# Kernel tuning notes

Hardware: AMD Instinct MI355X
Metric: run time of the kernel (lower is better)

## Reference

```python
import jax, jax.numpy as jnp
import numpy as np

NHEADS = 16


def setup_inputs() -> dict:
    key = jax.random.key(0)
    ks = jax.random.split(key, 5)
    B, S, D = 2, 2048, 1024
    x = jax.random.normal(ks[0], (B, S, D), dtype=jnp.float32)
    W_packed = jax.random.normal(ks[1], (3 * D, D), dtype=jnp.float32) * (1.0 / np.sqrt(D))
    b_packed = jax.random.normal(ks[2], (3 * D,), dtype=jnp.float32) * 0.02
    W_out = jax.random.normal(ks[3], (D, D), dtype=jnp.float32) * (1.0 / np.sqrt(D))
    b_out = jax.random.normal(ks[4], (D,), dtype=jnp.float32) * 0.02
    return {"x": x, "W_packed": W_packed, "b_packed": b_packed, "W_out": W_out, "b_out": b_out}


def reference(x, W_packed, b_packed, W_out, b_out):
    B, S, D = x.shape
    H = NHEADS
    hd = D // H
    # packed QKV projection (self-attention: q is k is v)
    qkv = x @ W_packed.T + b_packed                       # [B,S,3D]
    q, k, v = jnp.split(qkv, 3, axis=-1)

    def heads(t):
        return t.reshape(B, S, H, hd).transpose(0, 2, 1, 3)  # [B,H,S,hd]

    q, k, v = map(heads, (q, k, v))

    # ALiBi slopes per flex path: exp2(-(h+1)*8/H)
    slopes = jnp.exp2(-(jnp.arange(1, H + 1, dtype=x.dtype) * (8.0 / H)))  # [H]
    pos = jnp.arange(S)
    rel = (pos[None, :] - pos[:, None]).astype(x.dtype)    # kv_idx - q_idx, [S,S]
    bias = slopes[:, None, None] * rel                     # [H,S,S]
    causal = pos[None, :] <= pos[:, None]                  # allowed positions
    neg = jnp.finfo(x.dtype).min
    attn_mask = jnp.where(causal[None, :, :], bias, neg)   # [H,S,S]

    scale = 1.0 / np.sqrt(hd)
    scores = jnp.einsum("bhqd,bhkd->bhqk", q, k) * scale + attn_mask[None]
    attn = jax.nn.softmax(scores, axis=-1)
    out = jnp.einsum("bhqk,bhkd->bhqd", attn, v)           # [B,H,S,hd]
    out = out.transpose(0, 2, 1, 3).reshape(B, S, D)
    return out @ W_out.T + b_out
```

## Files before the change

### kernel.cpp

```cpp
#include <hip/hip_runtime.h>

typedef float f32x4 __attribute__((ext_vector_type(4)));
typedef __bf16 bf16x8 __attribute__((ext_vector_type(8)));
typedef unsigned short u16;

__device__ __forceinline__ f32x4 mfma16(bf16x8 a, bf16x8 b, f32x4 c) {
  return __builtin_amdgcn_mfma_f32_16x16x32_bf16(a, b, c, 0, 0, 0);
}

__device__ __forceinline__ int pidx16(int row, int kc) {
  return ((((row >> 6) * 32 + (kc >> 2)) * 4 + ((row >> 4) & 3)) << 6) +
         ((kc & 3) << 4) + (row & 15);
}

__global__ void cvt3_kernel(const float* __restrict__ x,
                            const float* __restrict__ wp,
                            const float* __restrict__ wo,
                            u16* __restrict__ apx, u16* __restrict__ bpx,
                            u16* __restrict__ wox) {
  int idx = blockIdx.x * blockDim.x + threadIdx.x;
  int stride = gridDim.x * blockDim.x;
  for (int i = idx; i < 1048576; i += stride) {
    const float* src;
    u16* dst;
    int j;
    if (i < 524288) {
      j = i; src = x + (size_t)j * 8; dst = apx;
    } else if (i < 917504) {
      j = i - 524288; src = wp + (size_t)j * 8; dst = bpx;
    } else {
      j = i - 917504; src = wo + (size_t)j * 8; dst = wox;
    }
    f32x4 a = *(const f32x4*)src;
    f32x4 b = *(const f32x4*)(src + 4);
    bf16x8 r;
#pragma unroll
    for (int e = 0; e < 4; ++e) {
      r[e] = (__bf16)a[e];
      r[4 + e] = (__bf16)b[e];
    }
    int row = j >> 7, kc = j & 127;
    *(bf16x8*)(dst + (size_t)pidx16(row, kc) * 8) = r;
  }
}

template <int NREP, int MODE>
__global__ __launch_bounds__(256, 2) void gemm_frag(
    const u16* __restrict__ apx, const u16* __restrict__ bpx,
    const float* __restrict__ bias, float* __restrict__ Cout,
    __bf16* __restrict__ qb, __bf16* __restrict__ kp, __bf16* __restrict__ vp,
    int N) {
  const int tid = threadIdx.x;
  const int wid = tid >> 6;
  const int lane = tid & 63;
  const int lr = lane & 15, lg = lane >> 4;

  const int lid = blockIdx.x;
  const int xcd = lid & 7;
  const int local = lid >> 3;
  const int mib = xcd * 2 + (local & 1);
  const int nj = local >> 1;
  const int mi64 = mib * 4 + wid;

  const u16* ab = apx + (size_t)mi64 * 65536 + lane * 8;
  const u16* bb;
  int colbase;
  if (NREP == 4) {
    bb = bpx + (size_t)nj * 65536 + lane * 8;
    colbase = nj * 64;
  } else {
    bb = bpx + (size_t)(nj >> 1) * 65536 + (nj & 1) * 1024 + lane * 8;
    colbase = nj * 32;
  }

  f32x4 acc[4][NREP] = {};
  bf16x8 a0[4], b0[NREP], a1[4], b1[NREP];
#pragma unroll
  for (int mt = 0; mt < 4; ++mt) a0[mt] = *(const bf16x8*)(ab + mt * 512);
#pragma unroll
  for (int nt = 0; nt < NREP; ++nt) b0[nt] = *(const bf16x8*)(bb + nt * 512);

  for (int kt = 0; kt < 32; kt += 2) {
#pragma unroll
    for (int mt = 0; mt < 4; ++mt)
      a1[mt] = *(const bf16x8*)(ab + (kt + 1) * 2048 + mt * 512);
#pragma unroll
    for (int nt = 0; nt < NREP; ++nt)
      b1[nt] = *(const bf16x8*)(bb + (kt + 1) * 2048 + nt * 512);
#pragma unroll
    for (int mt = 0; mt < 4; ++mt)
#pragma unroll
      for (int nt = 0; nt < NREP; ++nt)
        acc[mt][nt] = mfma16(a0[mt], b0[nt], acc[mt][nt]);
    if (kt + 2 < 32) {
#pragma unroll
      for (int mt = 0; mt < 4; ++mt)
        a0[mt] = *(const bf16x8*)(ab + (kt + 2) * 2048 + mt * 512);
#pragma unroll
      for (int nt = 0; nt < NREP; ++nt)
        b0[nt] = *(const bf16x8*)(bb + (kt + 2) * 2048 + nt * 512);
    }
#pragma unroll
    for (int mt = 0; mt < 4; ++mt)
#pragma unroll
      for (int nt = 0; nt < NREP; ++nt)
        acc[mt][nt] = mfma16(a1[mt], b1[nt], acc[mt][nt]);
  }

#pragma unroll
  for (int nt = 0; nt < NREP; ++nt) {
    int col = colbase + nt * 16 + lr;
    float bv = bias[col];
#pragma unroll
    for (int mt = 0; mt < 4; ++mt) {
#pragma unroll
      for (int r = 0; r < 4; ++r) {
        int row = mi64 * 64 + mt * 16 + lg * 4 + r;
        float val = acc[mt][nt][r] + bv;
        if (MODE == 0) {
          Cout[(size_t)row * N + col] = val;
        } else {
          __bf16 bx = (__bf16)val;
          int b = row >> 11, s = row & 2047;
          int third = col >> 10, hd = col & 1023;
          int h = hd >> 6, d = hd & 63;
          if (third == 0) {
            qb[(size_t)row * 1024 + hd] = bx;
          } else {
            int bh = b * 16 + h, t2 = s >> 6, sr = s & 63;
            size_t tb = ((size_t)(bh * 32 + t2)) * 4096;
            if (third == 1)
              kp[tb + (sr >> 4) * 1024 + (d >> 5) * 512 + ((d >> 3) & 3) * 128 +
                 (sr & 15) * 8 + (d & 7)] = bx;
            else
              vp[tb + (d >> 4) * 1024 + (sr >> 5) * 512 + ((sr >> 3) & 3) * 128 +
                 (d & 15) * 8 + (sr & 7)] = bx;
          }
        }
      }
    }
  }
}

__global__ __launch_bounds__(64, 4) void attn_kernel(
    const __bf16* __restrict__ qb, const __bf16* __restrict__ kp,
    const __bf16* __restrict__ vp, u16* __restrict__ abp) {
  __shared__ __bf16 p_lds[16][72];
  const int lane = threadIdx.x & 63;
  const int lr = lane & 15;
  const int lg = lane >> 4;

  const int lid = blockIdx.x;
  const int xcd = lid & 7;
  const int rest = lid >> 3;
  const int bh = xcd * 4 + (rest & 3);
  const int a16 = 127 - (rest >> 2);
  const int b = bh >> 4, h = bh & 15;
  const int qr0 = a16 * 16;
  const int ntl = (a16 >> 2) + 1;

  const float LOG2E = 1.4426950408889634f;
  const float c1 = 0.125f * LOG2E;
  const float c2 = exp2f(-(float)(h + 1) * 0.5f) * LOG2E;

  bf16x8 ones;
#pragma unroll
  for (int j = 0; j < 8; ++j) ones[j] = (__bf16)1.0f;

  const u16* ktiles = (const u16*)kp + (size_t)bh * 32 * 4096;
  const u16* vtiles = (const u16*)vp + (size_t)bh * 32 * 4096;

  const __bf16* qrow = qb + (size_t)(b * 2048 + qr0 + lr) * 1024 + h * 64;
  bf16x8 qf0 = *(const bf16x8*)(qrow + lg * 8);
  bf16x8 qf1 = *(const bf16x8*)(qrow + 32 + lg * 8);

  float m[4], l[4], cq[4];
  f32x4 o[4];
#pragma unroll
  for (int r = 0; r < 4; ++r) {
    m[r] = 0.f;
    l[r] = 0.f;
    cq[r] = c2 * (float)(qr0 + lg * 4 + r);
  }
#pragma unroll
  for (int dt = 0; dt < 4; ++dt) o[dt] = (f32x4){0.f, 0.f, 0.f, 0.f};

  for (int t = 0; t < ntl; ++t) {
    const u16* kb = ktiles + (size_t)t * 4096;
    const u16* vb = vtiles + (size_t)t * 4096;
    const int kv = t * 64;
    const bool last = (t == ntl - 1);

    bf16x8 ka[8], va[8];
#pragma unroll
    for (int j = 0; j < 8; ++j)
      ka[j] = *(const bf16x8*)(kb + j * 512 + lane * 8);
#pragma unroll
    for (int j = 0; j < 8; ++j)
      va[j] = *(const bf16x8*)(vb + j * 512 + lane * 8);

    f32x4 s[4];
#pragma unroll
    for (int nt = 0; nt < 4; ++nt) {
      f32x4 tt = (f32x4){0.f, 0.f, 0.f, 0.f};
      tt = mfma16(qf0, ka[nt * 2], tt);
      tt = mfma16(qf1, ka[nt * 2 + 1], tt);
      s[nt] = tt;
    }

#pragma unroll
    for (int nt = 0; nt < 4; ++nt) {
      float bnt = c2 * (float)(kv + nt * 16 + lr);
#pragma unroll
      for (int r = 0; r < 4; ++r)
        s[nt][r] = __builtin_fmaf(s[nt][r], c1, bnt - cq[r]);
    }
    if (last) {
#pragma unroll
      for (int nt = 0; nt < 4; ++nt) {
        float kf = (float)(kv + nt * 16 + lr);
#pragma unroll
        for (int r = 0; r < 4; ++r) {
          float qi = (float)(qr0 + lg * 4 + r);
          if (kf > qi) s[nt][r] = -1e30f;
        }
      }
    }

    float pm[4];
#pragma unroll
    for (int r = 0; r < 4; ++r)
      pm[r] = fmaxf(fmaxf(s[0][r], s[1][r]), fmaxf(s[2][r], s[3][r]));
    bool ok = (pm[0] <= m[0] + 8.f) && (pm[1] <= m[1] + 8.f) &&
              (pm[2] <= m[2] + 8.f) && (pm[3] <= m[3] + 8.f);
    if (!__all(ok)) {
#pragma unroll
      for (int r = 0; r < 4; ++r)
#pragma unroll
        for (int d = 1; d < 16; d <<= 1)
          pm[r] = fmaxf(pm[r], __shfl_xor(pm[r], d));
#pragma unroll
      for (int r = 0; r < 4; ++r) {
        float mn = fmaxf(m[r], pm[r]);
        float fac = __builtin_amdgcn_exp2f(m[r] - mn);
        m[r] = mn;
        l[r] *= fac;
#pragma unroll
        for (int dt = 0; dt < 4; ++dt) o[dt][r] *= fac;
      }
    }

#pragma unroll
    for (int nt = 0; nt < 4; ++nt)
#pragma unroll
      for (int r = 0; r < 4; ++r) {
        float e = __builtin_amdgcn_exp2f(s[nt][r] - m[r]);
        p_lds[lg * 4 + r][nt * 16 + lr] = (__bf16)e;
      }

    bf16x8 pa0 = *(const bf16x8*)&p_lds[lr][lg * 8];
    bf16x8 pa1 = *(const bf16x8*)&p_lds[lr][32 + lg * 8];

    {
      f32x4 tt = (f32x4){0.f, 0.f, 0.f, 0.f};
      tt = mfma16(pa0, ones, tt);
      tt = mfma16(pa1, ones, tt);
#pragma unroll
      for (int r = 0; r < 4; ++r) l[r] += tt[r];
    }

#pragma unroll
    for (int dt = 0; dt < 4; ++dt) {
      o[dt] = mfma16(pa0, va[dt * 2], o[dt]);
      o[dt] = mfma16(pa1, va[dt * 2 + 1], o[dt]);
    }
  }

  const int mi_g = b * 32 + (a16 >> 2);
#pragma unroll
  for (int dt = 0; dt < 4; ++dt)
#pragma unroll
    for (int r = 0; r < 4; ++r) {
      float val = o[dt][r] / l[r];
      __bf16 bx = (__bf16)val;
      int off16 = (((mi_g * 32 + h * 2 + (dt >> 1)) * 4 + (a16 & 3)) << 6) +
                  (((dt & 1) * 2 + (lr >> 3)) << 4) + lg * 4 + r;
      abp[(size_t)off16 * 8 + (lr & 7)] = *(u16*)&bx;
    }
}

extern "C" void kernel_launch(void* const* d_in, const int* in_sizes, int n_in,
                              void* d_out, int out_size, void* d_ws, size_t ws_size,
                              hipStream_t stream) {
  (void)in_sizes; (void)n_in; (void)out_size; (void)ws_size;
  const float* x = (const float*)d_in[0];
  const float* Wp = (const float*)d_in[1];
  const float* bp = (const float*)d_in[2];
  const float* Wo = (const float*)d_in[3];
  const float* bo = (const float*)d_in[4];
  float* out = (float*)d_out;

  char* ws = (char*)d_ws;
  u16* apx = (u16*)(ws);
  u16* bpx = (u16*)(ws + (size_t)(8u << 20));
  u16* wox = (u16*)(ws + (size_t)(14u << 20));
  u16* qbp = (u16*)(ws + (size_t)(16u << 20));
  u16* kpp = (u16*)(ws + (size_t)(24u << 20));
  u16* vpp = (u16*)(ws + (size_t)(32u << 20));
  u16* abp = (u16*)(ws + (size_t)(40u << 20));

  cvt3_kernel<<<2048, 256, 0, stream>>>(x, Wp, Wo, apx, bpx, wox);
  gemm_frag<4, 1><<<768, 256, 0, stream>>>(
      apx, bpx, bp, nullptr, (__bf16*)qbp, (__bf16*)kpp, (__bf16*)vpp, 3072);
  attn_kernel<<<4096, 64, 0, stream>>>(
      (const __bf16*)qbp, (const __bf16*)kpp, (const __bf16*)vpp, abp);
  gemm_frag<2, 0><<<512, 256, 0, stream>>>(
      abp, wox, bo, out, nullptr, nullptr, nullptr, 1024);
}
```

Before: 119.6 us.

## Replace QKV projection GEMM with LDS-staged 256x256 tiled kernel

The QKV projection GEMM moves from a register-only fragment-layout kernel to a 512-thread, 256x256-tile kernel. It stages A and B tiles into double-buffered LDS using global_load_lds with an XOR swizzle, and interleaves staging of quarter-tiles with four MFMA phases using barriers and setprio. The conversion kernel now writes x and W_packed as plain row-major bf16 instead of the pre-permuted fragment layout. The intent is more operand reuse per global byte and better overlap of loads with MFMA, at the cost of many more barriers and a grid of only 192 workgroups.

```diff
diff --git a/kernel.cpp b/kernel.cpp
--- a/kernel.cpp
+++ b/kernel.cpp
@@ -8,6 +8,12 @@
   return __builtin_amdgcn_mfma_f32_16x16x32_bf16(a, b, c, 0, 0, 0);
 }
 
+__device__ __forceinline__ void gll16(const void* g, void* l) {
+  __builtin_amdgcn_global_load_lds(
+      (const __attribute__((address_space(1))) void*)g,
+      (__attribute__((address_space(3))) void*)l, 16, 0, 0);
+}
+
 __device__ __forceinline__ int pidx16(int row, int kc) {
   return ((((row >> 6) * 32 + (kc >> 2)) * 4 + ((row >> 4) & 3)) << 6) +
          ((kc & 3) << 4) + (row & 15);
@@ -16,21 +22,17 @@
 __global__ void cvt3_kernel(const float* __restrict__ x,
                             const float* __restrict__ wp,
                             const float* __restrict__ wo,
-                            u16* __restrict__ apx, u16* __restrict__ bpx,
+                            __bf16* __restrict__ xb, __bf16* __restrict__ wpb,
                             u16* __restrict__ wox) {
   int idx = blockIdx.x * blockDim.x + threadIdx.x;
   int stride = gridDim.x * blockDim.x;
   for (int i = idx; i < 1048576; i += stride) {
     const float* src;
-    u16* dst;
     int j;
-    if (i < 524288) {
-      j = i; src = x + (size_t)j * 8; dst = apx;
-    } else if (i < 917504) {
-      j = i - 524288; src = wp + (size_t)j * 8; dst = bpx;
-    } else {
-      j = i - 917504; src = wo + (size_t)j * 8; dst = wox;
-    }
+    int mode;
+    if (i < 524288) { j = i; src = x + (size_t)j * 8; mode = 0; }
+    else if (i < 917504) { j = i - 524288; src = wp + (size_t)j * 8; mode = 1; }
+    else { j = i - 917504; src = wo + (size_t)j * 8; mode = 2; }
     f32x4 a = *(const f32x4*)src;
     f32x4 b = *(const f32x4*)(src + 4);
     bf16x8 r;
@@ -39,83 +41,173 @@
       r[e] = (__bf16)a[e];
       r[4 + e] = (__bf16)b[e];
     }
-    int row = j >> 7, kc = j & 127;
-    *(bf16x8*)(dst + (size_t)pidx16(row, kc) * 8) = r;
-  }
-}
-
-template <int NREP, int MODE>
-__global__ __launch_bounds__(256, 2) void gemm_frag(
-    const u16* __restrict__ apx, const u16* __restrict__ bpx,
+    if (mode == 0) *(bf16x8*)(xb + (size_t)j * 8) = r;
+    else if (mode == 1) *(bf16x8*)(wpb + (size_t)j * 8) = r;
+    else {
+      int row = j >> 7, kc = j & 127;
+      *(bf16x8*)(wox + (size_t)pidx16(row, kc) * 8) = r;
+    }
+  }
+}
+
+template <int MODE>
+__global__ __launch_bounds__(512, 2) void gemm8p(
+    const u16* __restrict__ A, const u16* __restrict__ B,
     const float* __restrict__ bias, float* __restrict__ Cout,
     __bf16* __restrict__ qb, __bf16* __restrict__ kp, __bf16* __restrict__ vp,
-    int N) {
+    int N, int K, int mtiles) {
+  __shared__ u16 lA[2 * 256 * 64];
+  __shared__ u16 lB[2 * 256 * 64];
   const int tid = threadIdx.x;
   const int wid = tid >> 6;
   const int lane = tid & 63;
   const int lr = lane & 15, lg = lane >> 4;
 
+  const int nwg = gridDim.x;
   const int lid = blockIdx.x;
-  const int xcd = lid & 7;
-  const int local = lid >> 3;
-  const int mib = xcd * 2 + (local & 1);
-  const int nj = local >> 1;
-  const int mi64 = mib * 4 + wid;
-
-  const u16* ab = apx + (size_t)mi64 * 65536 + lane * 8;
-  const u16* bb;
-  int colbase;
-  if (NREP == 4) {
-    bb = bpx + (size_t)nj * 65536 + lane * 8;
-    colbase = nj * 64;
-  } else {
-    bb = bpx + (size_t)(nj >> 1) * 65536 + (nj & 1) * 1024 + lane * 8;
-    colbase = nj * 32;
-  }
-
-  f32x4 acc[4][NREP] = {};
-  bf16x8 a0[4], b0[NREP], a1[4], b1[NREP];
-#pragma unroll
-  for (int mt = 0; mt < 4; ++mt) a0[mt] = *(const bf16x8*)(ab + mt * 512);
-#pragma unroll
-  for (int nt = 0; nt < NREP; ++nt) b0[nt] = *(const bf16x8*)(bb + nt * 512);
-
-  for (int kt = 0; kt < 32; kt += 2) {
-#pragma unroll
-    for (int mt = 0; mt < 4; ++mt)
-      a1[mt] = *(const bf16x8*)(ab + (kt + 1) * 2048 + mt * 512);
-#pragma unroll
-    for (int nt = 0; nt < NREP; ++nt)
-      b1[nt] = *(const bf16x8*)(bb + (kt + 1) * 2048 + nt * 512);
-#pragma unroll
-    for (int mt = 0; mt < 4; ++mt)
-#pragma unroll
-      for (int nt = 0; nt < NREP; ++nt)
-        acc[mt][nt] = mfma16(a0[mt], b0[nt], acc[mt][nt]);
-    if (kt + 2 < 32) {
-#pragma unroll
-      for (int mt = 0; mt < 4; ++mt)
-        a0[mt] = *(const bf16x8*)(ab + (kt + 2) * 2048 + mt * 512);
-#pragma unroll
-      for (int nt = 0; nt < NREP; ++nt)
-        b0[nt] = *(const bf16x8*)(bb + (kt + 2) * 2048 + nt * 512);
-    }
-#pragma unroll
-    for (int mt = 0; mt < 4; ++mt)
-#pragma unroll
-      for (int nt = 0; nt < NREP; ++nt)
-        acc[mt][nt] = mfma16(a1[mt], b1[nt], acc[mt][nt]);
-  }
-
-#pragma unroll
-  for (int nt = 0; nt < NREP; ++nt) {
-    int col = colbase + nt * 16 + lr;
+  const int sw = (lid & 7) * (nwg >> 3) + (lid >> 3);
+  const int bm = (sw % mtiles) * 256;
+  const int bn = (sw / mtiles) * 256;
+  const int wm = (wid >> 2) * 128;
+  const int wn = (wid & 3) * 64;
+
+  f32x4 acc[8][4] = {};
+  const int KT = K >> 6;
+  const int NH = KT * 4;
+
+  auto stageh = [&](int h) {
+    if (h >= NH) return;
+    const int kt = h >> 2, part = h & 3, slot = kt & 1;
+    const int kk = kt << 6;
+#pragma unroll
+    for (int j = 0; j < 2; ++j) {
+      int o16 = tid + j * 512;
+      int rl = o16 >> 3;
+      int gcol = (((o16 & 7) ^ (rl & 7)) << 3);
+      if (part < 2)
+        gll16(A + (size_t)(bm + part * 128 + rl) * K + kk + gcol,
+              (char*)lA + slot * 32768 + part * 16384 + o16 * 16);
+      else
+        gll16(B + (size_t)(bn + (part - 2) * 128 + rl) * K + kk + gcol,
+              (char*)lB + slot * 32768 + (part - 2) * 16384 + o16 * 16);
+    }
+  };
+
+  auto rdA = [&](int slot, int mt, int ks) -> bf16x8 {
+    int row = wm + mt * 16 + lr;
+    int col = ((ks * 4 + lg) ^ (row & 7)) << 3;
+    return *(const bf16x8*)&lA[slot * 16384 + row * 64 + col];
+  };
+  auto rdB = [&](int slot, int nt, int ks) -> bf16x8 {
+    int row = wn + nt * 16 + lr;
+    int col = ((ks * 4 + lg) ^ (row & 7)) << 3;
+    return *(const bf16x8*)&lB[slot * 16384 + row * 64 + col];
+  };
+
+#pragma unroll
+  for (int h = 0; h < 5; ++h) stageh(h);
+  asm volatile("s_waitcnt vmcnt(2)" ::: "memory");
+  __builtin_amdgcn_s_barrier();
+
+  bf16x8 afA[4][2], afB[4][2], bfA[2][2], bfB[2][2];
+  for (int kt = 0; kt < KT; ++kt) {
+    const int slot = kt & 1;
+    const int hb = (kt + 1) * 4;
+#pragma unroll
+    for (int mt = 0; mt < 4; ++mt) {
+      afA[mt][0] = rdA(slot, mt, 0);
+      afA[mt][1] = rdA(slot, mt, 1);
+    }
+#pragma unroll
+    for (int nt = 0; nt < 2; ++nt) {
+      bfA[nt][0] = rdB(slot, nt, 0);
+      bfA[nt][1] = rdB(slot, nt, 1);
+    }
+    stageh(hb + 1);
+    __builtin_amdgcn_sched_barrier(0);
+    __builtin_amdgcn_s_barrier();
+    asm volatile("s_waitcnt lgkmcnt(0)" ::: "memory");
+    __builtin_amdgcn_sched_barrier(0);
+    __builtin_amdgcn_s_setprio(1);
+#pragma unroll
+    for (int mt = 0; mt < 4; ++mt)
+#pragma unroll
+      for (int nt = 0; nt < 2; ++nt)
+#pragma unroll
+        for (int ks = 0; ks < 2; ++ks)
+          acc[mt][nt] = mfma16(afA[mt][ks], bfA[nt][ks], acc[mt][nt]);
+    __builtin_amdgcn_s_setprio(0);
+    __builtin_amdgcn_sched_barrier(0);
+    __builtin_amdgcn_s_barrier();
+#pragma unroll
+    for (int nt = 0; nt < 2; ++nt) {
+      bfB[nt][0] = rdB(slot, nt + 2, 0);
+      bfB[nt][1] = rdB(slot, nt + 2, 1);
+    }
+    stageh(hb + 2);
+    __builtin_amdgcn_sched_barrier(0);
+    __builtin_amdgcn_s_barrier();
+    asm volatile("s_waitcnt lgkmcnt(0)" ::: "memory");
+    __builtin_amdgcn_sched_barrier(0);
+    __builtin_amdgcn_s_setprio(1);
+#pragma unroll
+    for (int mt = 0; mt < 4; ++mt)
+#pragma unroll
+      for (int nt = 0; nt < 2; ++nt)
+#pragma unroll
+        for (int ks = 0; ks < 2; ++ks)
+          acc[mt][nt + 2] = mfma16(afA[mt][ks], bfB[nt][ks], acc[mt][nt + 2]);
+    __builtin_amdgcn_s_setprio(0);
+    __builtin_amdgcn_sched_barrier(0);
+    __builtin_amdgcn_s_barrier();
+#pragma unroll
+    for (int mt = 0; mt < 4; ++mt) {
+      afB[mt][0] = rdA(slot, mt + 4, 0);
+      afB[mt][1] = rdA(slot, mt + 4, 1);
+    }
+    stageh(hb + 3);
+    __builtin_amdgcn_sched_barrier(0);
+    __builtin_amdgcn_s_barrier();
+    asm volatile("s_waitcnt lgkmcnt(0)" ::: "memory");
+    __builtin_amdgcn_sched_barrier(0);
+    __builtin_amdgcn_s_setprio(1);
+#pragma unroll
+    for (int mt = 0; mt < 4; ++mt)
+#pragma unroll
+      for (int nt = 0; nt < 2; ++nt)
+#pragma unroll
+        for (int ks = 0; ks < 2; ++ks)
+          acc[mt + 4][nt] = mfma16(afB[mt][ks], bfA[nt][ks], acc[mt + 4][nt]);
+    __builtin_amdgcn_s_setprio(0);
+    __builtin_amdgcn_sched_barrier(0);
+    __builtin_amdgcn_s_barrier();
+    stageh(hb + 4);
+    __builtin_amdgcn_sched_barrier(0);
+    __builtin_amdgcn_s_barrier();
+    __builtin_amdgcn_s_setprio(1);
+#pragma unroll
+    for (int mt = 0; mt < 4; ++mt)
+#pragma unroll
+      for (int nt = 0; nt < 2; ++nt)
+#pragma unroll
+        for (int ks = 0; ks < 2; ++ks)
+          acc[mt + 4][nt + 2] =
+              mfma16(afB[mt][ks], bfB[nt][ks], acc[mt + 4][nt + 2]);
+    __builtin_amdgcn_s_setprio(0);
+    __builtin_amdgcn_sched_barrier(0);
+    asm volatile("s_waitcnt vmcnt(2)" ::: "memory");
+    __builtin_amdgcn_s_barrier();
+  }
+
+#pragma unroll
+  for (int nt = 0; nt < 4; ++nt) {
+    int col = bn + wn + nt * 16 + lr;
     float bv = bias[col];
 #pragma unroll
-    for (int mt = 0; mt < 4; ++mt) {
+    for (int mt = 0; mt < 8; ++mt) {
 #pragma unroll
       for (int r = 0; r < 4; ++r) {
-        int row = mi64 * 64 + mt * 16 + lg * 4 + r;
+        int row = bm + wm + mt * 16 + lg * 4 + r;
         float val = acc[mt][nt][r] + bv;
         if (MODE == 0) {
           Cout[(size_t)row * N + col] = val;
@@ -142,6 +234,82 @@
   }
 }
 
+template <int NREP, int MODE>
+__global__ __launch_bounds__(256, 2) void gemm_frag(
+    const u16* __restrict__ apx, const u16* __restrict__ bpx,
+    const float* __restrict__ bias, float* __restrict__ Cout, int N) {
+  const int tid = threadIdx.x;
+  const int wid = tid >> 6;
+  const int lane = tid & 63;
+  const int lr = lane & 15, lg = lane >> 4;
+
+  const int lid = blockIdx.x;
+  const int xcd = lid & 7;
+  const int local = lid >> 3;
+  const int mib = xcd * 2 + (local & 1);
+  const int nj = local >> 1;
+  const int mi64 = mib * 4 + wid;
+
+  const u16* ab = apx + (size_t)mi64 * 65536 + lane * 8;
+  const u16* bb;
+  int colbase;
+  if (NREP == 4) {
+    bb = bpx + (size_t)nj * 65536 + lane * 8;
+    colbase = nj * 64;
+  } else {
+    bb = bpx + (size_t)(nj >> 1) * 65536 + (nj & 1) * 1024 + lane * 8;
+    colbase = nj * 32;
+  }
+
+  f32x4 acc[4][NREP] = {};
+  bf16x8 a0[4], b0[NREP], a1[4], b1[NREP];
+#pragma unroll
+  for (int mt = 0; mt < 4; ++mt) a0[mt] = *(const bf16x8*)(ab + mt * 512);
+#pragma unroll
+  for (int nt = 0; nt < NREP; ++nt) b0[nt] = *(const bf16x8*)(bb + nt * 512);
+
+  for (int kt = 0; kt < 32; kt += 2) {
+#pragma unroll
+    for (int mt = 0; mt < 4; ++mt)
+      a1[mt] = *(const bf16x8*)(ab + (kt + 1) * 2048 + mt * 512);
+#pragma unroll
+    for (int nt = 0; nt < NREP; ++nt)
+      b1[nt] = *(const bf16x8*)(bb + (kt + 1) * 2048 + nt * 512);
+#pragma unroll
+    for (int mt = 0; mt < 4; ++mt)
+#pragma unroll
+      for (int nt = 0; nt < NREP; ++nt)
+        acc[mt][nt] = mfma16(a0[mt], b0[nt], acc[mt][nt]);
+    if (kt + 2 < 32) {
+#pragma unroll
+      for (int mt = 0; mt < 4; ++mt)
+        a0[mt] = *(const bf16x8*)(ab + (kt + 2) * 2048 + mt * 512);
+#pragma unroll
+      for (int nt = 0; nt < NREP; ++nt)
+        b0[nt] = *(const bf16x8*)(bb + (kt + 2) * 2048 + nt * 512);
+    }
+#pragma unroll
+    for (int mt = 0; mt < 4; ++mt)
+#pragma unroll
+      for (int nt = 0; nt < NREP; ++nt)
+        acc[mt][nt] = mfma16(a1[mt], b1[nt], acc[mt][nt]);
+  }
+
+#pragma unroll
+  for (int nt = 0; nt < NREP; ++nt) {
+    int col = colbase + nt * 16 + lr;
+    float bv = bias[col];
+#pragma unroll
+    for (int mt = 0; mt < 4; ++mt) {
+#pragma unroll
+      for (int r = 0; r < 4; ++r) {
+        int row = mi64 * 64 + mt * 16 + lg * 4 + r;
+        Cout[(size_t)row * N + col] = acc[mt][nt][r] + bv;
+      }
+    }
+  }
+}
+
 __global__ __launch_bounds__(64, 4) void attn_kernel(
     const __bf16* __restrict__ qb, const __bf16* __restrict__ kp,
     const __bf16* __restrict__ vp, u16* __restrict__ abp) {
@@ -301,19 +469,20 @@
   float* out = (float*)d_out;
 
   char* ws = (char*)d_ws;
-  u16* apx = (u16*)(ws);
-  u16* bpx = (u16*)(ws + (size_t)(8u << 20));
+  u16* xb  = (u16*)(ws);
+  u16* wpb = (u16*)(ws + (size_t)(8u << 20));
   u16* wox = (u16*)(ws + (size_t)(14u << 20));
   u16* qbp = (u16*)(ws + (size_t)(16u << 20));
   u16* kpp = (u16*)(ws + (size_t)(24u << 20));
   u16* vpp = (u16*)(ws + (size_t)(32u << 20));
   u16* abp = (u16*)(ws + (size_t)(40u << 20));
 
-  cvt3_kernel<<<2048, 256, 0, stream>>>(x, Wp, Wo, apx, bpx, wox);
-  gemm_frag<4, 1><<<768, 256, 0, stream>>>(
-      apx, bpx, bp, nullptr, (__bf16*)qbp, (__bf16*)kpp, (__bf16*)vpp, 3072);
+  cvt3_kernel<<<2048, 256, 0, stream>>>(x, Wp, Wo, (__bf16*)xb, (__bf16*)wpb,
+                                        wox);
+  gemm8p<1><<<192, 512, 0, stream>>>(
+      xb, wpb, bp, nullptr, (__bf16*)qbp, (__bf16*)kpp, (__bf16*)vpp,
+      3072, 1024, 16);
   attn_kernel<<<4096, 64, 0, stream>>>(
       (const __bf16*)qbp, (const __bf16*)kpp, (const __bf16*)vpp, abp);
-  gemm_frag<2, 0><<<512, 256, 0, stream>>>(
-      abp, wox, bo, out, nullptr, nullptr, nullptr, 1024);
-}
+  gemm_frag<2, 0><<<512, 256, 0, stream>>>(abp, wox, bo, out, 1024);
+}
```

Result: slower. 122.0 us (+2.0%).
